# Kernel optimization log

Measured on AMD Instinct MI355X. Metric: run time of the kernel, lower is better.

## Reference

```python
import jax, jax.numpy as jnp
import numpy as np
import math

B, S, H = 2, 2048, 2048
NH, HD = 16, 128           # num_heads, head_dim; num_kv_heads == num_heads (MHA)
THETA = 10000.0


def setup_inputs() -> dict:
    key = jax.random.key(0)
    ks = jax.random.split(key, 5)
    scale = 0.02
    hidden_states = jax.random.normal(ks[0], (B, S, H), jnp.float32)
    q_w = jax.random.normal(ks[1], (H, H), jnp.float32) * scale
    k_w = jax.random.normal(ks[2], (H, H), jnp.float32) * scale
    v_w = jax.random.normal(ks[3], (H, H), jnp.float32) * scale
    o_w = jax.random.normal(ks[4], (H, H), jnp.float32) * scale
    # additive causal mask, finite large-negative (as HF builds it)
    causal = jnp.tril(jnp.ones((S, S), bool))
    attention_mask = jnp.where(causal, 0.0, -1e9).astype(jnp.float32)[None, None]  # [1,1,S,S]
    position_ids = jnp.broadcast_to(jnp.arange(S, dtype=jnp.int64), (B, S))
    return {
        "hidden_states": hidden_states,
        "q_w": q_w, "k_w": k_w, "v_w": v_w, "o_w": o_w,
        "attention_mask": attention_mask,
        "position_ids": position_ids,
    }


def _rotate_half(x):
    x1, x2 = x[..., : x.shape[-1] // 2], x[..., x.shape[-1] // 2 :]
    return jnp.concatenate((-x2, x1), axis=-1)


def _rope_cos_sin(position_ids):
    inv_freq = 1.0 / (THETA ** (jnp.arange(0, HD, 2, dtype=jnp.float32) / HD))  # [HD/2]
    freqs = position_ids.astype(jnp.float32)[:, :, None] * inv_freq[None, None, :]  # [B,S,HD/2]
    emb = jnp.concatenate((freqs, freqs), axis=-1)  # [B,S,HD]
    # unsqueeze head dim (unsqueeze_dim=1 after transpose to [B,H,S,D])
    return jnp.cos(emb)[:, None], jnp.sin(emb)[:, None]  # [B,1,S,HD]


def reference(hidden_states, q_w, k_w, v_w, o_w, attention_mask, position_ids):
    # projections (torch Linear: y = x @ W^T), split heads -> [B,NH,S,HD]
    def proj(w):
        return jnp.einsum('bsh,oh->bso', hidden_states, w).reshape(B, S, NH, HD).transpose(0, 2, 1, 3)
    q, k, v = proj(q_w), proj(k_w), proj(v_w)

    cos, sin = _rope_cos_sin(position_ids)
    q = q * cos + _rotate_half(q) * sin
    k = k * cos + _rotate_half(k) * sin

    scores = jnp.einsum('bhqd,bhkd->bhqk', q, k) / math.sqrt(HD)  # [B,NH,S,S]
    scores = scores + attention_mask
    attn = jax.nn.softmax(scores, axis=-1)  # dropout p=0.0 -> identity
    out = jnp.einsum('bhqk,bhkd->bhqd', attn, v)  # [B,NH,S,HD]
    out = out.transpose(0, 2, 1, 3).reshape(B, S, H)
    return jnp.einsum('bsh,oh->bso', out, o_w)
```

## Files before the change

### kernel.cpp

```cpp
#include <hip/hip_runtime.h>
#include <hip/hip_bf16.h>

using bf16 = __hip_bfloat16;
typedef short  short8  __attribute__((ext_vector_type(8)));
typedef float  float4_ __attribute__((ext_vector_type(4)));
typedef int    int4_   __attribute__((ext_vector_type(4)));

typedef __attribute__((address_space(1))) const void* gas_ptr;
typedef __attribute__((address_space(3))) void*       las_ptr;

#define MFMA_BF16(a, b, c) __builtin_amdgcn_mfma_f32_16x16x32_bf16((a), (b), (c), 0, 0, 0)

__device__ __forceinline__ float bf2f(bf16 v) { return __bfloat162float(v); }
__device__ __forceinline__ bf16  f2bf(float v) { return __float2bfloat16(v); }

#define BAR() do { asm volatile("" ::: "memory"); __builtin_amdgcn_s_barrier(); asm volatile("" ::: "memory"); } while (0)
#define WAITLGKM0() asm volatile("s_waitcnt lgkmcnt(0)" ::: "memory")

__global__ __launch_bounds__(256)
void cvt_all(const float* __restrict__ X,  const float* __restrict__ Wq,
             const float* __restrict__ Wk, const float* __restrict__ Wv,
             const float* __restrict__ Wo,
             bf16* __restrict__ Xb,  bf16* __restrict__ Wqb,
             bf16* __restrict__ Wkb, bf16* __restrict__ Wvb,
             bf16* __restrict__ Wob)
{
    const size_t i = ((size_t)blockIdx.x * 256 + threadIdx.x) * 8;
    const float* src; bf16* dst; size_t off;
    if (i < 8388608)       { src = X;  dst = Xb;  off = i; }
    else if (i < 12582912) { src = Wq; dst = Wqb; off = i - 8388608; }
    else if (i < 16777216) { src = Wk; dst = Wkb; off = i - 12582912; }
    else if (i < 20971520) { src = Wv; dst = Wvb; off = i - 16777216; }
    else                   { src = Wo; dst = Wob; off = i - 20971520; }
    const float4_ a = *(const float4_*)(src + off);
    const float4_ b = *(const float4_*)(src + off + 4);
    union { short8 s; bf16 h[8]; } u;
#pragma unroll
    for (int j = 0; j < 4; ++j) { u.h[j] = f2bf(a[j]); u.h[j + 4] = f2bf(b[j]); }
    *(short8*)(dst + off) = u.s;
}

__global__ __launch_bounds__(512, 2)
void gemm_bn128(const bf16* __restrict__ Ap, const bf16* __restrict__ Wp,
                bf16* __restrict__ Oq, float* __restrict__ OF, int mode)
{
    constexpr int NT = 32;
    __shared__ bf16 As0[2 * 256 * 64];
    __shared__ bf16 Bs0[2 * 128 * 64];

    const int nwg  = gridDim.x * gridDim.y;
    const int bid0 = blockIdx.y * gridDim.x + blockIdx.x;
    const int cpx  = nwg >> 3;
    const int swzb = (bid0 & 7) * cpx + (bid0 >> 3);
    const int bn = (swzb % gridDim.x) * 128;
    const int bm = (swzb / gridDim.x) * 256;

    const int tid  = threadIdx.x;
    const int w    = tid >> 6;
    const int ln   = tid & 63;
    const int r15  = ln & 15;
    const int quad = ln >> 4;
    const int wr   = w >> 1;
    const int wc   = w & 1;

    const int srow = ln >> 3;
    const int scol = ((ln & 7) ^ srow) * 8;
    const int w8   = w * 8;
    const int cx   = (r15 & 7) * 8;

#define STAGE_A(pb, ts) do {                                                \
    _Pragma("unroll")                                                       \
    for (int c = 0; c < 4; ++c) {                                           \
        const int rl = c * 64 + w8;                                         \
        __builtin_amdgcn_global_load_lds(                                   \
            (gas_ptr)(Ap + (size_t)(bm + rl + srow) * 2048 + (ts) * 64 + scol), \
            (las_ptr)(As0 + (pb) * 16384 + rl * 64), 16, 0, 0);             \
    } } while (0)

#define STAGE_B0(pb, ts) do {                                               \
    const int rl = w8;                                                      \
    __builtin_amdgcn_global_load_lds(                                       \
        (gas_ptr)(Wp + (size_t)(bn + rl + srow) * 2048 + (ts) * 64 + scol), \
        (las_ptr)(Bs0 + (pb) * 8192 + rl * 64), 16, 0, 0);                  \
    } while (0)

#define STAGE_B1(pb, ts) do {                                               \
    const int rl = 64 + w8;                                                 \
    __builtin_amdgcn_global_load_lds(                                       \
        (gas_ptr)(Wp + (size_t)(bn + rl + srow) * 2048 + (ts) * 64 + scol), \
        (las_ptr)(Bs0 + (pb) * 8192 + rl * 64), 16, 0, 0);                  \
    } while (0)

#define LDA() do {                                                          \
    _Pragma("unroll")                                                       \
    for (int mi = 0; mi < 4; ++mi) {                                        \
        const int row = wr * 64 + mi * 16 + r15;                            \
        a[mi][0] = *(const short8*)(As0 + p * 16384 + row * 64 + ((quad * 8) ^ cx));      \
        a[mi][1] = *(const short8*)(As0 + p * 16384 + row * 64 + ((32 + quad * 8) ^ cx)); \
    } } while (0)

#define LDB(qn) do {                                                        \
    _Pragma("unroll")                                                       \
    for (int j = 0; j < 2; ++j) {                                           \
        const int row = wc * 64 + ((qn) * 2 + j) * 16 + r15;                \
        b[j][0] = *(const short8*)(Bs0 + p * 8192 + row * 64 + ((quad * 8) ^ cx));      \
        b[j][1] = *(const short8*)(Bs0 + p * 8192 + row * 64 + ((32 + quad * 8) ^ cx)); \
    } } while (0)

#define MM(qn) do {                                                         \
    __builtin_amdgcn_s_setprio(1);                                          \
    _Pragma("unroll")                                                       \
    for (int mi = 0; mi < 4; ++mi)                                          \
        _Pragma("unroll")                                                   \
        for (int j = 0; j < 2; ++j)                                         \
            _Pragma("unroll")                                               \
            for (int kk = 0; kk < 2; ++kk)                                  \
                acc[mi][(qn) * 2 + j] =                                     \
                    MFMA_BF16(a[mi][kk], b[j][kk], acc[mi][(qn) * 2 + j]);  \
    __builtin_amdgcn_s_setprio(0); } while (0)

    float4_ acc[4][4];
    const float4_ fzero = {0.f, 0.f, 0.f, 0.f};
#pragma unroll
    for (int i = 0; i < 4; ++i)
#pragma unroll
        for (int j = 0; j < 4; ++j) acc[i][j] = fzero;

    short8 a[4][2], b[2][2];

    STAGE_A(0, 0); STAGE_B0(0, 0); STAGE_B1(0, 0);
    STAGE_A(1, 1); STAGE_B0(1, 1);
    asm volatile("s_waitcnt vmcnt(5)" ::: "memory");
    BAR();

    for (int t = 0; t < NT; ++t) {
        const int p = t & 1, pq = p ^ 1;
        LDA(); LDB(0);
        if (t + 1 < NT) STAGE_B1(pq, t + 1);
        asm volatile("s_waitcnt lgkmcnt(8)" ::: "memory");
        BAR(); WAITLGKM0();
        MM(0);
        BAR();
        LDB(1);
        if (t + 2 < NT) { STAGE_A(p, t + 2); STAGE_B0(p, t + 2); }
        BAR(); WAITLGKM0();
        MM(1);
        if (t >= NT - 2) { asm volatile("s_waitcnt vmcnt(0)" ::: "memory"); }
        else             { asm volatile("s_waitcnt vmcnt(5)" ::: "memory"); }
        BAR();
    }

#pragma unroll
    for (int mi = 0; mi < 4; ++mi) {
#pragma unroll
        for (int ni = 0; ni < 4; ++ni) {
#pragma unroll
            for (int r = 0; r < 4; ++r) {
                const int row = bm + wr * 64 + mi * 16 + quad * 4 + r;
                const int col = bn + wc * 64 + ni * 16 + r15;
                const float v = acc[mi][ni][r];
                if (mode == 0) {
                    const int z = col >> 11, c2 = col & 2047;
                    const int h = c2 >> 7, d = c2 & 127;
                    const int bb = row >> 11, s = row & 2047;
                    Oq[(size_t)z * 8388608 + (((size_t)bb * 16 + h) * 2048 + s) * 128 + d] = f2bf(v);
                } else {
                    OF[(size_t)row * 2048 + col] = v;
                }
            }
        }
    }
#undef STAGE_A
#undef STAGE_B0
#undef STAGE_B1
#undef LDA
#undef LDB
#undef MM
}

__global__ __launch_bounds__(256)
void rope_scale(bf16* __restrict__ Q, bf16* __restrict__ Kb)
{
    const int idx = blockIdx.x * 256 + threadIdx.x;
    const int d  = idx & 63;
    const int s  = (idx >> 6) & 2047;
    const int bh = idx >> 17;
    const size_t base = ((size_t)bh * 2048 + s) * 128;

    const float inv_freq = expf(-(float)d * (9.210340371976184f / 64.f));
    const float ang = (float)s * inv_freq;
    const float c = cosf(ang), sn = sinf(ang);
    const float sc = 0.08838834764831845f;

    const float q1 = bf2f(Q[base + d]), q2 = bf2f(Q[base + d + 64]);
    Q[base + d]      = f2bf((q1 * c - q2 * sn) * sc);
    Q[base + d + 64] = f2bf((q2 * c + q1 * sn) * sc);

    const float k1 = bf2f(Kb[base + d]), k2 = bf2f(Kb[base + d + 64]);
    Kb[base + d]      = f2bf(k1 * c - k2 * sn);
    Kb[base + d + 64] = f2bf(k2 * c + k1 * sn);
}

__global__ __launch_bounds__(512)
void flash_attn(const bf16* __restrict__ Qg, const bf16* __restrict__ Kg,
                const bf16* __restrict__ Vg, bf16* __restrict__ Og)
{
    constexpr int S = 2048;
    const int qb = blockIdx.x;
    const int bh = blockIdx.y;
    const int b = bh >> 4, h = bh & 15;
    const size_t base = (size_t)bh * S * 128;
    const bf16* Qp = Qg + base;
    const bf16* Kp = Kg + base;
    const bf16* Vp = Vg + base;

    const int tid  = threadIdx.x;
    const int wave = tid >> 6;
    const int ln   = tid & 63;
    const int r15  = ln & 15;
    const int quad = ln >> 4;

    __shared__ bf16 Ks[64][136];
    __shared__ bf16 Vt[128][72];
    __shared__ bf16 Ps[8][16][72];

    const int qs    = qb * 128;
    const int qrow0 = qs + wave * 16;
    const int dt    = qrow0 >> 6;
    const int ktmax = 2 * qb + 1;

    short8 qf[4];
#pragma unroll
    for (int ks = 0; ks < 4; ++ks)
        qf[ks] = *(const short8*)&Qp[(size_t)(qrow0 + r15) * 128 + ks * 32 + quad * 8];

    float4_ acc_o[8];
    const float4_ fzero = {0.f, 0.f, 0.f, 0.f};
#pragma unroll
    for (int of = 0; of < 8; ++of) acc_o[of] = fzero;
    float m_run[4], l_run[4];
#pragma unroll
    for (int r = 0; r < 4; ++r) { m_run[r] = -__builtin_inff(); l_run[r] = 0.f; }

    const int kr = tid >> 4;
    const int kc = (tid & 15) * 8;
    const int vd = wave * 16;

    {
#pragma unroll
        for (int p = 0; p < 2; ++p)
            *(int4_*)&Ks[kr + p * 32][kc] =
                *(const int4_*)&Kp[(size_t)(kr + p * 32) * 128 + kc];
        union { int4_ v; bf16 h[8]; } u;
#pragma unroll
        for (int p = 0; p < 2; ++p) {
            u.v = *(const int4_*)&Vp[(size_t)ln * 128 + vd + p * 8];
#pragma unroll
            for (int j = 0; j < 8; ++j)
                Vt[vd + p * 8 + j][ln] = u.h[j];
        }
    }
    __syncthreads();

    for (int kt = 0; kt <= ktmax; ++kt) {
        const bool more = (kt < ktmax);

        int4_ kpre0, kpre1, vpre0, vpre1;
        if (more) {
            const int krow = (kt + 1) * 64;
            kpre0 = *(const int4_*)&Kp[(size_t)(krow + kr) * 128 + kc];
            kpre1 = *(const int4_*)&Kp[(size_t)(krow + kr + 32) * 128 + kc];
            vpre0 = *(const int4_*)&Vp[(size_t)(krow + ln) * 128 + vd];
            vpre1 = *(const int4_*)&Vp[(size_t)(krow + ln) * 128 + vd + 8];
        }

        if (kt <= dt) {
            float4_ sacc[4];
            __builtin_amdgcn_s_setprio(1);
#pragma unroll
            for (int nf = 0; nf < 4; ++nf) {
                sacc[nf] = fzero;
#pragma unroll
                for (int ks = 0; ks < 4; ++ks) {
                    short8 kf = *(const short8*)&Ks[nf * 16 + r15][ks * 32 + quad * 8];
                    sacc[nf] = MFMA_BF16(qf[ks], kf, sacc[nf]);
                }
            }
            __builtin_amdgcn_s_setprio(0);

            if (kt == dt) {
                const int ro = (qrow0 & 63) + quad * 4;
#pragma unroll
                for (int nf = 0; nf < 4; ++nf) {
                    const int col = nf * 16 + r15;
#pragma unroll
                    for (int r = 0; r < 4; ++r)
                        if (col > ro + r) sacc[nf][r] = -__builtin_inff();
                }
            }

            float mnew[4], alpha[4];
#pragma unroll
            for (int r = 0; r < 4; ++r) {
                float rm = fmaxf(fmaxf(sacc[0][r], sacc[1][r]),
                                 fmaxf(sacc[2][r], sacc[3][r]));
                rm = fmaxf(rm, __shfl_xor(rm, 1));
                rm = fmaxf(rm, __shfl_xor(rm, 2));
                rm = fmaxf(rm, __shfl_xor(rm, 4));
                rm = fmaxf(rm, __shfl_xor(rm, 8));
                mnew[r]  = fmaxf(m_run[r], rm);
                alpha[r] = __expf(m_run[r] - mnew[r]);
                m_run[r] = mnew[r];
            }
            float rs[4] = {0.f, 0.f, 0.f, 0.f};
#pragma unroll
            for (int nf = 0; nf < 4; ++nf) {
#pragma unroll
                for (int r = 0; r < 4; ++r) {
                    const float p = __expf(sacc[nf][r] - mnew[r]);
                    rs[r] += p;
                    Ps[wave][quad * 4 + r][nf * 16 + r15] = f2bf(p);
                }
            }
#pragma unroll
            for (int r = 0; r < 4; ++r) {
                float t = rs[r];
                t += __shfl_xor(t, 1);
                t += __shfl_xor(t, 2);
                t += __shfl_xor(t, 4);
                t += __shfl_xor(t, 8);
                l_run[r] = l_run[r] * alpha[r] + t;
            }
#pragma unroll
            for (int of = 0; of < 8; ++of)
#pragma unroll
                for (int r = 0; r < 4; ++r)
                    acc_o[of][r] *= alpha[r];

            __builtin_amdgcn_s_setprio(1);
#pragma unroll
            for (int k2 = 0; k2 < 2; ++k2) {
                short8 pf = *(const short8*)&Ps[wave][r15][k2 * 32 + quad * 8];
#pragma unroll
                for (int of = 0; of < 8; ++of) {
                    short8 vf = *(const short8*)&Vt[of * 16 + r15][k2 * 32 + quad * 8];
                    acc_o[of] = MFMA_BF16(pf, vf, acc_o[of]);
                }
            }
            __builtin_amdgcn_s_setprio(0);
        }

        __syncthreads();
        if (more) {
            *(int4_*)&Ks[kr][kc]      = kpre0;
            *(int4_*)&Ks[kr + 32][kc] = kpre1;
            union { int4_ v; bf16 h[8]; } u;
            u.v = vpre0;
#pragma unroll
            for (int j = 0; j < 8; ++j) Vt[vd + j][ln] = u.h[j];
            u.v = vpre1;
#pragma unroll
            for (int j = 0; j < 8; ++j) Vt[vd + 8 + j][ln] = u.h[j];
        }
        __syncthreads();
    }

#pragma unroll
    for (int r = 0; r < 4; ++r) {
        const float inv = 1.f / l_run[r];
        const int  s  = qrow0 + quad * 4 + r;
        const size_t ob = (((size_t)b * S + s) * 16 + h) * 128;
#pragma unroll
        for (int of = 0; of < 8; ++of)
            Og[ob + of * 16 + r15] = f2bf(acc_o[of][r] * inv);
    }
}

extern "C" void kernel_launch(void* const* d_in, const int* in_sizes, int n_in,
                              void* d_out, int out_size, void* d_ws, size_t ws_size,
                              hipStream_t stream)
{
    const float* X  = (const float*)d_in[0];
    const float* Wq = (const float*)d_in[1];
    const float* Wk = (const float*)d_in[2];
    const float* Wv = (const float*)d_in[3];
    const float* Wo = (const float*)d_in[4];
    float* out = (float*)d_out;

    bf16* Xb  = (bf16*)d_ws;
    bf16* Wqb = Xb  + 8388608;
    bf16* Wkb = Wqb + 4194304;
    bf16* Wvb = Wkb + 4194304;
    bf16* Wob = Wvb + 4194304;
    bf16* q   = Wob + 4194304;
    bf16* k   = q   + 8388608;
    bf16* v   = k   + 8388608;
    bf16* ao  = v   + 8388608;

    dim3 blk(256);
    cvt_all<<<dim3(12288), blk, 0, stream>>>(X, Wq, Wk, Wv, Wo,
                                             Xb, Wqb, Wkb, Wvb, Wob);
    gemm_bn128<<<dim3(48, 16), dim3(512), 0, stream>>>(Xb, Wqb, q, nullptr, 0);
    rope_scale<<<dim3((2 * 16 * 2048 * 64) / 256), blk, 0, stream>>>(q, k);
    flash_attn<<<dim3(16, 32), dim3(512), 0, stream>>>(q, k, v, ao);
    gemm_bn128<<<dim3(16, 16), dim3(512), 0, stream>>>(ao, Wob, nullptr, out, 1);
}
```

Measured before the change: 462.0 us.

## Pair low and high causal query blocks per workgroup to balance attention work

Each flash-attention workgroup now processes two query blocks, pr and 15-pr, so every workgroup does roughly equal causal work. K/V tiles loaded once are shared by both query strips, and the grid halves to 8x32 blocks. This removes the triangular load imbalance and reduces redundant K/V loads for low blocks. The cost is doubled accumulator register state per thread, which may lower occupancy or cause spills, and there are fewer workgroups (256) on a machine with many CUs.

```diff
diff --git a/kernel.cpp b/kernel.cpp
--- a/kernel.cpp
+++ b/kernel.cpp
@@ -201,12 +201,95 @@
     Kb[base + d + 64] = f2bf(k2 * c + k1 * sn);
 }
 
+__device__ __forceinline__ void fa_strip_step(
+    const bf16 (* __restrict__ Ks)[136], const bf16 (* __restrict__ Vt)[72],
+    bf16 (* __restrict__ PsW)[72],
+    const short8 qf[4], float4_ acc_o[8], float m_run[4], float l_run[4],
+    int kt, int dt, int qrow0, int r15, int quad)
+{
+    if (kt > dt) return;
+    const float4_ fzero = {0.f, 0.f, 0.f, 0.f};
+    float4_ sacc[4];
+    __builtin_amdgcn_s_setprio(1);
+#pragma unroll
+    for (int nf = 0; nf < 4; ++nf) {
+        sacc[nf] = fzero;
+#pragma unroll
+        for (int ks = 0; ks < 4; ++ks) {
+            short8 kf = *(const short8*)&Ks[nf * 16 + r15][ks * 32 + quad * 8];
+            sacc[nf] = MFMA_BF16(qf[ks], kf, sacc[nf]);
+        }
+    }
+    __builtin_amdgcn_s_setprio(0);
+
+    if (kt == dt) {
+        const int ro = (qrow0 & 63) + quad * 4;
+#pragma unroll
+        for (int nf = 0; nf < 4; ++nf) {
+            const int col = nf * 16 + r15;
+#pragma unroll
+            for (int r = 0; r < 4; ++r)
+                if (col > ro + r) sacc[nf][r] = -__builtin_inff();
+        }
+    }
+
+    float mnew[4], alpha[4];
+#pragma unroll
+    for (int r = 0; r < 4; ++r) {
+        float rm = fmaxf(fmaxf(sacc[0][r], sacc[1][r]),
+                         fmaxf(sacc[2][r], sacc[3][r]));
+        rm = fmaxf(rm, __shfl_xor(rm, 1));
+        rm = fmaxf(rm, __shfl_xor(rm, 2));
+        rm = fmaxf(rm, __shfl_xor(rm, 4));
+        rm = fmaxf(rm, __shfl_xor(rm, 8));
+        mnew[r]  = fmaxf(m_run[r], rm);
+        alpha[r] = __expf(m_run[r] - mnew[r]);
+        m_run[r] = mnew[r];
+    }
+    float rs[4] = {0.f, 0.f, 0.f, 0.f};
+#pragma unroll
+    for (int nf = 0; nf < 4; ++nf) {
+#pragma unroll
+        for (int r = 0; r < 4; ++r) {
+            const float pp = __expf(sacc[nf][r] - mnew[r]);
+            rs[r] += pp;
+            PsW[quad * 4 + r][nf * 16 + r15] = f2bf(pp);
+        }
+    }
+#pragma unroll
+    for (int r = 0; r < 4; ++r) {
+        float t = rs[r];
+        t += __shfl_xor(t, 1);
+        t += __shfl_xor(t, 2);
+        t += __shfl_xor(t, 4);
+        t += __shfl_xor(t, 8);
+        l_run[r] = l_run[r] * alpha[r] + t;
+    }
+#pragma unroll
+    for (int of = 0; of < 8; ++of)
+#pragma unroll
+        for (int r = 0; r < 4; ++r)
+            acc_o[of][r] *= alpha[r];
+
+    __builtin_amdgcn_s_setprio(1);
+#pragma unroll
+    for (int k2 = 0; k2 < 2; ++k2) {
+        short8 pf = *(const short8*)&PsW[r15][k2 * 32 + quad * 8];
+#pragma unroll
+        for (int of = 0; of < 8; ++of) {
+            short8 vf = *(const short8*)&Vt[of * 16 + r15][k2 * 32 + quad * 8];
+            acc_o[of] = MFMA_BF16(pf, vf, acc_o[of]);
+        }
+    }
+    __builtin_amdgcn_s_setprio(0);
+}
+
 __global__ __launch_bounds__(512)
 void flash_attn(const bf16* __restrict__ Qg, const bf16* __restrict__ Kg,
                 const bf16* __restrict__ Vg, bf16* __restrict__ Og)
 {
     constexpr int S = 2048;
-    const int qb = blockIdx.x;
+    const int pr = blockIdx.x;
     const int bh = blockIdx.y;
     const int b = bh >> 4, h = bh & 15;
     const size_t base = (size_t)bh * S * 128;
@@ -224,23 +307,29 @@
     __shared__ bf16 Vt[128][72];
     __shared__ bf16 Ps[8][16][72];
 
-    const int qs    = qb * 128;
-    const int qrow0 = qs + wave * 16;
-    const int dt    = qrow0 >> 6;
-    const int ktmax = 2 * qb + 1;
-
-    short8 qf[4];
-#pragma unroll
-    for (int ks = 0; ks < 4; ++ks)
-        qf[ks] = *(const short8*)&Qp[(size_t)(qrow0 + r15) * 128 + ks * 32 + quad * 8];
-
-    float4_ acc_o[8];
+    const int qlo0 = pr * 128 + wave * 16;
+    const int qhi0 = (15 - pr) * 128 + wave * 16;
+    const int dtlo = qlo0 >> 6;
+    const int dthi = qhi0 >> 6;
+    const int ktmax = 2 * (15 - pr) + 1;
+
+    short8 qflo[4], qfhi[4];
+#pragma unroll
+    for (int ks = 0; ks < 4; ++ks) {
+        qflo[ks] = *(const short8*)&Qp[(size_t)(qlo0 + r15) * 128 + ks * 32 + quad * 8];
+        qfhi[ks] = *(const short8*)&Qp[(size_t)(qhi0 + r15) * 128 + ks * 32 + quad * 8];
+    }
+
+    float4_ acc_lo[8], acc_hi[8];
     const float4_ fzero = {0.f, 0.f, 0.f, 0.f};
 #pragma unroll
-    for (int of = 0; of < 8; ++of) acc_o[of] = fzero;
-    float m_run[4], l_run[4];
-#pragma unroll
-    for (int r = 0; r < 4; ++r) { m_run[r] = -__builtin_inff(); l_run[r] = 0.f; }
+    for (int of = 0; of < 8; ++of) { acc_lo[of] = fzero; acc_hi[of] = fzero; }
+    float m_lo[4], l_lo[4], m_hi[4], l_hi[4];
+#pragma unroll
+    for (int r = 0; r < 4; ++r) {
+        m_lo[r] = -__builtin_inff(); l_lo[r] = 0.f;
+        m_hi[r] = -__builtin_inff(); l_hi[r] = 0.f;
+    }
 
     const int kr = tid >> 4;
     const int kc = (tid & 15) * 8;
@@ -274,81 +363,10 @@
             vpre1 = *(const int4_*)&Vp[(size_t)(krow + ln) * 128 + vd + 8];
         }
 
-        if (kt <= dt) {
-            float4_ sacc[4];
-            __builtin_amdgcn_s_setprio(1);
-#pragma unroll
-            for (int nf = 0; nf < 4; ++nf) {
-                sacc[nf] = fzero;
-#pragma unroll
-                for (int ks = 0; ks < 4; ++ks) {
-                    short8 kf = *(const short8*)&Ks[nf * 16 + r15][ks * 32 + quad * 8];
-                    sacc[nf] = MFMA_BF16(qf[ks], kf, sacc[nf]);
-                }
-            }
-            __builtin_amdgcn_s_setprio(0);
-
-            if (kt == dt) {
-                const int ro = (qrow0 & 63) + quad * 4;
-#pragma unroll
-                for (int nf = 0; nf < 4; ++nf) {
-                    const int col = nf * 16 + r15;
-#pragma unroll
-                    for (int r = 0; r < 4; ++r)
-                        if (col > ro + r) sacc[nf][r] = -__builtin_inff();
-                }
-            }
-
-            float mnew[4], alpha[4];
-#pragma unroll
-            for (int r = 0; r < 4; ++r) {
-                float rm = fmaxf(fmaxf(sacc[0][r], sacc[1][r]),
-                                 fmaxf(sacc[2][r], sacc[3][r]));
-                rm = fmaxf(rm, __shfl_xor(rm, 1));
-                rm = fmaxf(rm, __shfl_xor(rm, 2));
-                rm = fmaxf(rm, __shfl_xor(rm, 4));
-                rm = fmaxf(rm, __shfl_xor(rm, 8));
-                mnew[r]  = fmaxf(m_run[r], rm);
-                alpha[r] = __expf(m_run[r] - mnew[r]);
-                m_run[r] = mnew[r];
-            }
-            float rs[4] = {0.f, 0.f, 0.f, 0.f};
-#pragma unroll
-            for (int nf = 0; nf < 4; ++nf) {
-#pragma unroll
-                for (int r = 0; r < 4; ++r) {
-                    const float p = __expf(sacc[nf][r] - mnew[r]);
-                    rs[r] += p;
-                    Ps[wave][quad * 4 + r][nf * 16 + r15] = f2bf(p);
-                }
-            }
-#pragma unroll
-            for (int r = 0; r < 4; ++r) {
-                float t = rs[r];
-                t += __shfl_xor(t, 1);
-                t += __shfl_xor(t, 2);
-                t += __shfl_xor(t, 4);
-                t += __shfl_xor(t, 8);
-                l_run[r] = l_run[r] * alpha[r] + t;
-            }
-#pragma unroll
-            for (int of = 0; of < 8; ++of)
-#pragma unroll
-                for (int r = 0; r < 4; ++r)
-                    acc_o[of][r] *= alpha[r];
-
-            __builtin_amdgcn_s_setprio(1);
-#pragma unroll
-            for (int k2 = 0; k2 < 2; ++k2) {
-                short8 pf = *(const short8*)&Ps[wave][r15][k2 * 32 + quad * 8];
-#pragma unroll
-                for (int of = 0; of < 8; ++of) {
-                    short8 vf = *(const short8*)&Vt[of * 16 + r15][k2 * 32 + quad * 8];
-                    acc_o[of] = MFMA_BF16(pf, vf, acc_o[of]);
-                }
-            }
-            __builtin_amdgcn_s_setprio(0);
-        }
+        fa_strip_step(Ks, Vt, Ps[wave], qflo, acc_lo, m_lo, l_lo,
+                      kt, dtlo, qlo0, r15, quad);
+        fa_strip_step(Ks, Vt, Ps[wave], qfhi, acc_hi, m_hi, l_hi,
+                      kt, dthi, qhi0, r15, quad);
 
         __syncthreads();
         if (more) {
@@ -367,12 +385,21 @@
 
 #pragma unroll
     for (int r = 0; r < 4; ++r) {
-        const float inv = 1.f / l_run[r];
-        const int  s  = qrow0 + quad * 4 + r;
+        const float invl = 1.f / l_lo[r];
+        const int  s  = qlo0 + quad * 4 + r;
         const size_t ob = (((size_t)b * S + s) * 16 + h) * 128;
 #pragma unroll
         for (int of = 0; of < 8; ++of)
-            Og[ob + of * 16 + r15] = f2bf(acc_o[of][r] * inv);
+            Og[ob + of * 16 + r15] = f2bf(acc_lo[of][r] * invl);
+    }
+#pragma unroll
+    for (int r = 0; r < 4; ++r) {
+        const float invh = 1.f / l_hi[r];
+        const int  s  = qhi0 + quad * 4 + r;
+        const size_t ob = (((size_t)b * S + s) * 16 + h) * 128;
+#pragma unroll
+        for (int of = 0; of < 8; ++of)
+            Og[ob + of * 16 + r15] = f2bf(acc_hi[of][r] * invh);
     }
 }
 
@@ -402,6 +429,6 @@
                                              Xb, Wqb, Wkb, Wvb, Wob);
     gemm_bn128<<<dim3(48, 16), dim3(512), 0, stream>>>(Xb, Wqb, q, nullptr, 0);
     rope_scale<<<dim3((2 * 16 * 2048 * 64) / 256), blk, 0, stream>>>(q, k);
-    flash_attn<<<dim3(16, 32), dim3(512), 0, stream>>>(q, k, v, ao);
+    flash_attn<<<dim3(8, 32), dim3(512), 0, stream>>>(q, k, v, ao);
     gemm_bn128<<<dim3(16, 16), dim3(512), 0, stream>>>(ao, Wob, nullptr, out, 1);
 }
```

New measurement: 426.3 us. 7.7% less time.

## Pair causal query strips per block and give each wave 32 query rows

Applied to the files above, without the earlier changes.

Each flash-attention block now handles two 128-row query strips, strip pr and strip 15-pr, so every block does a balanced amount of causal work, and the grid is halved. Each wave processes 32 query rows using two MFMA row fragments, which reuses each K and V LDS fragment twice and doubles the work per shared-memory load. The cost is more registers per thread (two sets of accumulators and Q fragments) and a larger P buffer. Waves on the shorter strip sit idle for the later K tiles, and the grid now has only 256 blocks, so occupancy and the number of blocks in flight drop.

```diff
diff --git a/kernel.cpp b/kernel.cpp
--- a/kernel.cpp
+++ b/kernel.cpp
@@ -206,7 +206,7 @@
                 const bf16* __restrict__ Vg, bf16* __restrict__ Og)
 {
     constexpr int S = 2048;
-    const int qb = blockIdx.x;
+    const int pr = blockIdx.x;
     const int bh = blockIdx.y;
     const int b = bh >> 4, h = bh & 15;
     const size_t base = (size_t)bh * S * 128;
@@ -219,28 +219,37 @@
     const int ln   = tid & 63;
     const int r15  = ln & 15;
     const int quad = ln >> 4;
+    const int sid  = wave & 3;
+    const int hi   = wave >> 2;
 
     __shared__ bf16 Ks[64][136];
     __shared__ bf16 Vt[128][72];
-    __shared__ bf16 Ps[8][16][72];
-
-    const int qs    = qb * 128;
-    const int qrow0 = qs + wave * 16;
+    __shared__ bf16 Ps[8][32][72];
+
+    const int strip = hi ? (15 - pr) : pr;
+    const int qrow0 = strip * 128 + sid * 32;
     const int dt    = qrow0 >> 6;
-    const int ktmax = 2 * qb + 1;
-
-    short8 qf[4];
-#pragma unroll
-    for (int ks = 0; ks < 4; ++ks)
-        qf[ks] = *(const short8*)&Qp[(size_t)(qrow0 + r15) * 128 + ks * 32 + quad * 8];
-
-    float4_ acc_o[8];
+    const int ktmax = 2 * (15 - pr) + 1;
+
+    short8 qf[2][4];
+#pragma unroll
+    for (int rf = 0; rf < 2; ++rf)
+#pragma unroll
+        for (int ks = 0; ks < 4; ++ks)
+            qf[rf][ks] = *(const short8*)&Qp[(size_t)(qrow0 + rf * 16 + r15) * 128
+                                             + ks * 32 + quad * 8];
+
+    float4_ acc_o[2][8];
     const float4_ fzero = {0.f, 0.f, 0.f, 0.f};
 #pragma unroll
-    for (int of = 0; of < 8; ++of) acc_o[of] = fzero;
-    float m_run[4], l_run[4];
-#pragma unroll
-    for (int r = 0; r < 4; ++r) { m_run[r] = -__builtin_inff(); l_run[r] = 0.f; }
+    for (int rf = 0; rf < 2; ++rf)
+#pragma unroll
+        for (int of = 0; of < 8; ++of) acc_o[rf][of] = fzero;
+    float m_run[2][4], l_run[2][4];
+#pragma unroll
+    for (int rf = 0; rf < 2; ++rf)
+#pragma unroll
+        for (int r = 0; r < 4; ++r) { m_run[rf][r] = -__builtin_inff(); l_run[rf][r] = 0.f; }
 
     const int kr = tid >> 4;
     const int kc = (tid & 15) * 8;
@@ -275,76 +284,86 @@
         }
 
         if (kt <= dt) {
-            float4_ sacc[4];
+            float4_ sacc[2][4];
             __builtin_amdgcn_s_setprio(1);
 #pragma unroll
             for (int nf = 0; nf < 4; ++nf) {
-                sacc[nf] = fzero;
+                sacc[0][nf] = fzero;
+                sacc[1][nf] = fzero;
 #pragma unroll
                 for (int ks = 0; ks < 4; ++ks) {
                     short8 kf = *(const short8*)&Ks[nf * 16 + r15][ks * 32 + quad * 8];
-                    sacc[nf] = MFMA_BF16(qf[ks], kf, sacc[nf]);
+                    sacc[0][nf] = MFMA_BF16(qf[0][ks], kf, sacc[0][nf]);
+                    sacc[1][nf] = MFMA_BF16(qf[1][ks], kf, sacc[1][nf]);
                 }
             }
             __builtin_amdgcn_s_setprio(0);
 
             if (kt == dt) {
-                const int ro = (qrow0 & 63) + quad * 4;
+#pragma unroll
+                for (int rf = 0; rf < 2; ++rf) {
+                    const int ro = (qrow0 & 63) + rf * 16 + quad * 4;
+#pragma unroll
+                    for (int nf = 0; nf < 4; ++nf) {
+                        const int col = nf * 16 + r15;
+#pragma unroll
+                        for (int r = 0; r < 4; ++r)
+                            if (col > ro + r) sacc[rf][nf][r] = -__builtin_inff();
+                    }
+                }
+            }
+
+#pragma unroll
+            for (int rf = 0; rf < 2; ++rf) {
+                float mnew[4], alpha[4];
+#pragma unroll
+                for (int r = 0; r < 4; ++r) {
+                    float rm = fmaxf(fmaxf(sacc[rf][0][r], sacc[rf][1][r]),
+                                     fmaxf(sacc[rf][2][r], sacc[rf][3][r]));
+                    rm = fmaxf(rm, __shfl_xor(rm, 1));
+                    rm = fmaxf(rm, __shfl_xor(rm, 2));
+                    rm = fmaxf(rm, __shfl_xor(rm, 4));
+                    rm = fmaxf(rm, __shfl_xor(rm, 8));
+                    mnew[r]  = fmaxf(m_run[rf][r], rm);
+                    alpha[r] = __expf(m_run[rf][r] - mnew[r]);
+                    m_run[rf][r] = mnew[r];
+                }
+                float rs[4] = {0.f, 0.f, 0.f, 0.f};
 #pragma unroll
                 for (int nf = 0; nf < 4; ++nf) {
-                    const int col = nf * 16 + r15;
+#pragma unroll
+                    for (int r = 0; r < 4; ++r) {
+                        const float pp = __expf(sacc[rf][nf][r] - mnew[r]);
+                        rs[r] += pp;
+                        Ps[wave][rf * 16 + quad * 4 + r][nf * 16 + r15] = f2bf(pp);
+                    }
+                }
+#pragma unroll
+                for (int r = 0; r < 4; ++r) {
+                    float t = rs[r];
+                    t += __shfl_xor(t, 1);
+                    t += __shfl_xor(t, 2);
+                    t += __shfl_xor(t, 4);
+                    t += __shfl_xor(t, 8);
+                    l_run[rf][r] = l_run[rf][r] * alpha[r] + t;
+                }
+#pragma unroll
+                for (int of = 0; of < 8; ++of)
 #pragma unroll
                     for (int r = 0; r < 4; ++r)
-                        if (col > ro + r) sacc[nf][r] = -__builtin_inff();
-                }
+                        acc_o[rf][of][r] *= alpha[r];
             }
 
-            float mnew[4], alpha[4];
-#pragma unroll
-            for (int r = 0; r < 4; ++r) {
-                float rm = fmaxf(fmaxf(sacc[0][r], sacc[1][r]),
-                                 fmaxf(sacc[2][r], sacc[3][r]));
-                rm = fmaxf(rm, __shfl_xor(rm, 1));
-                rm = fmaxf(rm, __shfl_xor(rm, 2));
-                rm = fmaxf(rm, __shfl_xor(rm, 4));
-                rm = fmaxf(rm, __shfl_xor(rm, 8));
-                mnew[r]  = fmaxf(m_run[r], rm);
-                alpha[r] = __expf(m_run[r] - mnew[r]);
-                m_run[r] = mnew[r];
-            }
-            float rs[4] = {0.f, 0.f, 0.f, 0.f};
-#pragma unroll
-            for (int nf = 0; nf < 4; ++nf) {
-#pragma unroll
-                for (int r = 0; r < 4; ++r) {
-                    const float p = __expf(sacc[nf][r] - mnew[r]);
-                    rs[r] += p;
-                    Ps[wave][quad * 4 + r][nf * 16 + r15] = f2bf(p);
-                }
-            }
-#pragma unroll
-            for (int r = 0; r < 4; ++r) {
-                float t = rs[r];
-                t += __shfl_xor(t, 1);
-                t += __shfl_xor(t, 2);
-                t += __shfl_xor(t, 4);
-                t += __shfl_xor(t, 8);
-                l_run[r] = l_run[r] * alpha[r] + t;
-            }
-#pragma unroll
-            for (int of = 0; of < 8; ++of)
-#pragma unroll
-                for (int r = 0; r < 4; ++r)
-                    acc_o[of][r] *= alpha[r];
-
             __builtin_amdgcn_s_setprio(1);
 #pragma unroll
             for (int k2 = 0; k2 < 2; ++k2) {
-                short8 pf = *(const short8*)&Ps[wave][r15][k2 * 32 + quad * 8];
+                short8 pf0 = *(const short8*)&Ps[wave][r15][k2 * 32 + quad * 8];
+                short8 pf1 = *(const short8*)&Ps[wave][16 + r15][k2 * 32 + quad * 8];
 #pragma unroll
                 for (int of = 0; of < 8; ++of) {
                     short8 vf = *(const short8*)&Vt[of * 16 + r15][k2 * 32 + quad * 8];
-                    acc_o[of] = MFMA_BF16(pf, vf, acc_o[of]);
+                    acc_o[0][of] = MFMA_BF16(pf0, vf, acc_o[0][of]);
+                    acc_o[1][of] = MFMA_BF16(pf1, vf, acc_o[1][of]);
                 }
             }
             __builtin_amdgcn_s_setprio(0);
@@ -366,13 +385,16 @@
     }
 
 #pragma unroll
-    for (int r = 0; r < 4; ++r) {
-        const float inv = 1.f / l_run[r];
-        const int  s  = qrow0 + quad * 4 + r;
-        const size_t ob = (((size_t)b * S + s) * 16 + h) * 128;
-#pragma unroll
-        for (int of = 0; of < 8; ++of)
-            Og[ob + of * 16 + r15] = f2bf(acc_o[of][r] * inv);
+    for (int rf = 0; rf < 2; ++rf) {
+#pragma unroll
+        for (int r = 0; r < 4; ++r) {
+            const float inv = 1.f / l_run[rf][r];
+            const int  s  = qrow0 + rf * 16 + quad * 4 + r;
+            const size_t ob = (((size_t)b * S + s) * 16 + h) * 128;
+#pragma unroll
+            for (int of = 0; of < 8; ++of)
+                Og[ob + of * 16 + r15] = f2bf(acc_o[rf][of][r] * inv);
+        }
     }
 }
 
@@ -402,6 +424,6 @@
                                              Xb, Wqb, Wkb, Wvb, Wob);
     gemm_bn128<<<dim3(48, 16), dim3(512), 0, stream>>>(Xb, Wqb, q, nullptr, 0);
     rope_scale<<<dim3((2 * 16 * 2048 * 64) / 256), blk, 0, stream>>>(q, k);
-    flash_attn<<<dim3(16, 32), dim3(512), 0, stream>>>(q, k, v, ao);
+    flash_attn<<<dim3(8, 32), dim3(512), 0, stream>>>(q, k, v, ao);
     gemm_bn128<<<dim3(16, 16), dim3(512), 0, stream>>>(ao, Wob, nullptr, out, 1);
 }
```

After: 440.1 us. -4.7%, faster.
